# Optimization experiments

Measured on AMD Instinct MI355X. Metric: run time of the kernel, lower is better.

## Reference

```python
import jax, jax.numpy as jnp
import numpy as np

B, L, D_IN, D, P, NL = 8, 4096, 64, 512, 512, 3
EPS = 1e-5


def _ln(x, w, b):
    m = x.mean(-1, keepdims=True)
    v = ((x - m) ** 2).mean(-1, keepdims=True)
    return (x - m) * jax.lax.rsqrt(v + EPS) * w + b


def _gelu(x):
    return jax.nn.gelu(x, approximate=False)  # torch default = exact erf GELU


def _s5_scan(u, lam_re, lam_im, Bre, Bim, Cre, Cim, Dp, log_step):
    # u: (L, D). Diagonal complex SSM with ZOH discretization.
    lam = lam_re + 1j * lam_im                      # (P,)
    step = jnp.exp(log_step)                        # (P,)
    lam_bar = jnp.exp(lam * step)                   # (P,)
    Bt = Bre + 1j * Bim                             # (P, D)
    B_bar = ((lam_bar - 1.0) / lam)[:, None] * Bt   # (P, D)
    Bu = u.astype(jnp.complex64) @ B_bar.T          # (L, P)
    A = jnp.broadcast_to(lam_bar, Bu.shape)         # (L, P)

    def binop(a, b):
        A1, b1 = a
        A2, b2 = b
        return (A2 * A1, A2 * b1 + b2)

    _, xs = jax.lax.associative_scan(binop, (A, Bu))  # (L, P) states
    Ct = Cre + 1j * Cim                               # (D, P)
    return 2.0 * jnp.real(xs @ Ct.T) + Dp * u          # (L, D)


def setup_inputs() -> dict:
    key = jax.random.key(0)
    ks = iter(jax.random.split(key, 32))
    r = lambda s, sc=1.0: sc * jax.random.normal(next(ks), s, dtype=jnp.float32)
    inp = {}
    inp['x'] = r((B, L, D_IN))
    inp['lengths'] = jax.random.randint(next(ks), (B,), 1, L + 1, dtype=jnp.int32)
    inp['enc_w'] = r((D_IN, D), 0.05)
    inp['enc_b'] = jnp.zeros((D,), jnp.float32)
    # S5 SSM params per layer (stacked over NL)
    inp['lam_re'] = -jnp.exp(r((NL, P), 0.5))          # stable: Re(Lambda) < 0
    inp['lam_im'] = np.pi * r((NL, P))
    inp['Bre'] = r((NL, P, D), 1.0 / np.sqrt(D))
    inp['Bim'] = r((NL, P, D), 1.0 / np.sqrt(D))
    inp['Cre'] = r((NL, D, P), 1.0 / np.sqrt(P))
    inp['Cim'] = r((NL, D, P), 1.0 / np.sqrt(P))
    inp['Dp'] = r((NL, D))
    inp['log_step'] = jax.random.uniform(next(ks), (NL, P), jnp.float32, np.log(1e-3), np.log(1e-1))
    # S5Block norms and GEGLU FFN (ff_enc: D->2D no bias, ff_dec: D->D no bias)
    inp['an_w'] = jnp.ones((NL, D), jnp.float32)
    inp['an_b'] = jnp.zeros((NL, D), jnp.float32)
    inp['fn_w'] = jnp.ones((NL, D), jnp.float32)
    inp['fn_b'] = jnp.zeros((NL, D), jnp.float32)
    inp['ffe_w'] = r((NL, 2 * D, D), 1.0 / np.sqrt(D))
    inp['ffd_w'] = r((NL, D, D), 1.0 / np.sqrt(D))
    # outer prenorm LayerNorms
    inp['norm_w'] = jnp.ones((NL, D), jnp.float32)
    inp['norm_b'] = jnp.zeros((NL, D), jnp.float32)
    inp['head_w'] = r((1, D), 0.05)
    inp['head_b'] = jnp.zeros((1,), jnp.float32)
    return inp


def reference(x, lengths, enc_w, enc_b, lam_re, lam_im, Bre, Bim, Cre, Cim, Dp,
              log_step, an_w, an_b, fn_w, fn_b, ffe_w, ffd_w, norm_w, norm_b,
              head_w, head_b):
    h = x @ enc_w + enc_b  # (B, L, D)
    s5_b = jax.vmap(_s5_scan, in_axes=(0, None, None, None, None, None, None, None, None))
    for i in range(NL):
        z = _ln(h, norm_w[i], norm_b[i])  # prenorm (dropout = identity in eval)
        # --- S5Block ---
        fx = _ln(z, an_w[i], an_b[i])
        z = _gelu(s5_b(fx, lam_re[i], lam_im[i], Bre[i], Bim[i], Cre[i], Cim[i], Dp[i], log_step[i])) + fx
        fx = _ln(z, fn_w[i], fn_b[i])
        e = fx @ ffe_w[i].T                      # (B, L, 2D)
        a, g = jnp.split(e, 2, axis=-1)
        z = (a * _gelu(g)) @ ffd_w[i].T + fx      # GEGLU + residual
        h = h + z
    mask = (jnp.arange(L)[None, :] < lengths[:, None])[..., None]  # (B, L, 1)
    pooled = (h * mask).sum(axis=1) / jnp.maximum(lengths, 1)[:, None].astype(h.dtype)
    return (pooled @ head_w.T + head_b).squeeze(-1)  # (B,)
```

## Files before the change

kernel.cpp:

```cpp
#include <hip/hip_runtime.h>
#include <hip/hip_bf16.h>
#include <stdint.h>

#define BB 8
#define LL 4096
#define D_IN 64
#define DD 512
#define PP 512
#define NL 3
#define MTOK (BB * LL)
#define SCHUNK 128
#define NCHUNK (LL / SCHUNK)

typedef __bf16 bf16x8 __attribute__((ext_vector_type(8)));
typedef __bf16 bf16x4 __attribute__((ext_vector_type(4)));
typedef float f32x4 __attribute__((ext_vector_type(4)));

typedef const __attribute__((address_space(1))) void gvoid_t;
typedef __attribute__((address_space(3))) void svoid_t;

__device__ __forceinline__ void async16(const __bf16* g, __bf16* l) {
    __builtin_amdgcn_global_load_lds((gvoid_t*)g, (svoid_t*)l, 16, 0, 0);
}

__device__ __forceinline__ float gelu_f(float x) {
    return 0.5f * x * (1.0f + erff(x * 0.70710678118654752440f));
}
__device__ __forceinline__ float wred(float v) {
#pragma unroll
    for (int o = 32; o > 0; o >>= 1) v += __shfl_xor(v, o, 64);
    return v;
}
__device__ __forceinline__ float bflo(uint32_t u) { return __builtin_bit_cast(float, (uint32_t)(u << 16)); }
__device__ __forceinline__ float bfhi(uint32_t u) { return __builtin_bit_cast(float, (uint32_t)(u & 0xffff0000u)); }
__device__ __forceinline__ uint32_t packbf2(float a, float b) {
    unsigned short ha = __builtin_bit_cast(unsigned short, (__bf16)a);
    unsigned short hb = __builtin_bit_cast(unsigned short, (__bf16)b);
    return (uint32_t)ha | ((uint32_t)hb << 16);
}
__device__ __forceinline__ float ldf(const void* p, long i, int f) {
    return f ? ((const float*)p)[i] : (float)((const __bf16*)p)[i];
}
__device__ __forceinline__ void split1(float v, __bf16& h, __bf16& l) {
    h = (__bf16)v;
    l = (__bf16)(v - (float)h);
}

__global__ void detect(const uint32_t* __restrict__ an_w_raw, int* __restrict__ flag) {
    if (threadIdx.x == 0) *flag = (an_w_raw[0] == 0x3F800000u) ? 1 : 0;
}

template <bool AL, bool BL>
__device__ __forceinline__ void gemm_kloop(
    const __bf16* __restrict__ Ah, const __bf16* __restrict__ Al,
    const __bf16* __restrict__ Bh, const __bf16* __restrict__ Bl,
    long ga, long gb, int lda, int K,
    __bf16* dAh, __bf16* dAl, __bf16* dBh, __bf16* dBl,
    const __bf16* sAh, const __bf16* sAl, const __bf16* sBh, const __bf16* sBl,
    int wm, int wn, int fr, int co, f32x4 (&acc)[4][4])
{
    constexpr int HB = 16384;

    auto stage = [&](int boff, int k0) {
        async16(Ah + ga + k0, dAh + boff);
        async16(Ah + ga + k0 + 16 * (long)lda, dAh + boff + 512);
        if constexpr (AL) {
            async16(Al + ga + k0, dAl + boff);
            async16(Al + ga + k0 + 16 * (long)lda, dAl + boff + 512);
        }
        async16(Bh + gb + k0, dBh + boff);
        async16(Bh + gb + k0 + 16 * (long)K, dBh + boff + 512);
        if constexpr (BL) {
            async16(Bl + gb + k0, dBl + boff);
            async16(Bl + gb + k0 + 16 * (long)K, dBl + boff + 512);
        }
    };

    stage(0, 0);
    asm volatile("s_waitcnt vmcnt(0)" ::: "memory");
    __builtin_amdgcn_s_barrier();
    __builtin_amdgcn_sched_barrier(0);

    int roff = 0;
    for (int k0 = 0; k0 < K; k0 += 32) {
        if (k0 + 32 < K) stage(roff ^ HB, k0 + 32);

        bf16x8 afh[4], afl[4], bfh[4], bfl[4];
#pragma unroll
        for (int i = 0; i < 4; i++) {
            afh[i] = *(const bf16x8*)(sAh + roff + (wm * 64 + i * 16 + fr) * 32 + co);
            bfh[i] = *(const bf16x8*)(sBh + roff + (wn * 64 + i * 16 + fr) * 32 + co);
            if constexpr (AL) afl[i] = *(const bf16x8*)(sAl + roff + (wm * 64 + i * 16 + fr) * 32 + co);
            if constexpr (BL) bfl[i] = *(const bf16x8*)(sBl + roff + (wn * 64 + i * 16 + fr) * 32 + co);
        }
#pragma unroll
        for (int i = 0; i < 4; i++)
#pragma unroll
            for (int j = 0; j < 4; j++) {
                if constexpr (BL)
                    acc[i][j] = __builtin_amdgcn_mfma_f32_16x16x32_bf16(afh[i], bfl[j], acc[i][j], 0, 0, 0);
                if constexpr (AL)
                    acc[i][j] = __builtin_amdgcn_mfma_f32_16x16x32_bf16(afl[i], bfh[j], acc[i][j], 0, 0, 0);
                acc[i][j] = __builtin_amdgcn_mfma_f32_16x16x32_bf16(afh[i], bfh[j], acc[i][j], 0, 0, 0);
            }

        asm volatile("s_waitcnt vmcnt(0) lgkmcnt(0)" ::: "memory");
        __builtin_amdgcn_s_barrier();
        __builtin_amdgcn_sched_barrier(0);
        roff ^= HB;
    }
}

template <int MODE, bool ARAW, bool BRAW>
__global__ __launch_bounds__(256) void gemm_bt(
    const __bf16* __restrict__ Ah, const __bf16* __restrict__ Al, int lda,
    const __bf16* __restrict__ Bh, const __bf16* __restrict__ Bl,
    int M, int N, int K,
    __bf16* outh, __bf16* outl, float* h32,
    __bf16* fxh, __bf16* fxl, const float* __restrict__ vec,
    const int* __restrict__ lengths, float* __restrict__ partials, int b0,
    const int* __restrict__ flag)
{
    __shared__ __attribute__((aligned(16))) char smem[65536];
    __bf16* sAh = (__bf16*)smem;
    __bf16* sAl = (__bf16*)(smem + 8192);
    __bf16* sBh = (__bf16*)(smem + 16384);
    __bf16* sBl = (__bf16*)(smem + 24576);

    const int tid = threadIdx.x;
    const int lane = tid & 63;
    const int wave = tid >> 6;
    const int wm = wave & 1, wn = wave >> 1;
    const long m0 = (long)blockIdx.x * 128;
    const long n0 = (long)blockIdx.y * 128;

    f32x4 acc[4][4] = {};

    const int sr = lane >> 2;
    const int sc = ((lane & 3) ^ ((sr >> 1) & 3)) * 8;
    const long ga = (m0 + wave * 32 + sr) * (long)lda + sc;
    const long gb = (n0 + wave * 32 + sr) * (long)K + sc;
    __bf16* dAh = sAh + wave * 1024;
    __bf16* dAl = sAl + wave * 1024;
    __bf16* dBh = sBh + wave * 1024;
    __bf16* dBl = sBl + wave * 1024;

    const int fr = lane & 15;
    const int co = ((lane >> 4) ^ ((fr >> 1) & 3)) * 8;

    if constexpr (!ARAW && !BRAW) {
        gemm_kloop<true, true>(Ah, Al, Bh, Bl, ga, gb, lda, K, dAh, dAl, dBh, dBl,
                               sAh, sAl, sBh, sBl, wm, wn, fr, co, acc);
    } else {
        const int f32ds = *flag;
        if (f32ds) {
            gemm_kloop<true, true>(Ah, Al, Bh, Bl, ga, gb, lda, K, dAh, dAl, dBh, dBl,
                                   sAh, sAl, sBh, sBl, wm, wn, fr, co, acc);
        } else if constexpr (ARAW && BRAW) {
            gemm_kloop<false, false>(Ah, Al, Bh, Bl, ga, gb, lda, K, dAh, dAl, dBh, dBl,
                                     sAh, sAl, sBh, sBl, wm, wn, fr, co, acc);
        } else if constexpr (!ARAW && BRAW) {
            gemm_kloop<true, false>(Ah, Al, Bh, Bl, ga, gb, lda, K, dAh, dAl, dBh, dBl,
                                    sAh, sAl, sBh, sBl, wm, wn, fr, co, acc);
        } else {
            gemm_kloop<false, true>(Ah, Al, Bh, Bl, ga, gb, lda, K, dAh, dAl, dBh, dBl,
                                    sAh, sAl, sBh, sBl, wm, wn, fr, co, acc);
        }
    }

    float* scratch = (float*)smem + wave * 1088;
    const int er = (lane >> 4) * 4;
    const int ec = lane & 15;
    const int lr_rd = lane >> 3;
    const int lc_rd = (lane & 7) * 8;

    float pacc = 0.f;
    int lenb = 0;
    if (MODE == 5) lenb = lengths[b0 + (int)(blockIdx.x >> 5)];

#pragma unroll
    for (int i = 0; i < 4; i++) {
#pragma unroll
        for (int j = 0; j < 4; j++)
#pragma unroll
            for (int r = 0; r < 4; r++)
                scratch[(er + r) * 68 + j * 16 + ec] = acc[i][j][r];
#pragma unroll
        for (int s = 0; s < 2; s++) {
            const int lr = s * 8 + lr_rd;
            float v8[8];
            *(f32x4*)v8       = *(const f32x4*)&scratch[lr * 68 + lc_rd];
            *(f32x4*)(v8 + 4) = *(const f32x4*)&scratch[lr * 68 + lc_rd + 4];
            const long gm = m0 + wm * 64 + i * 16 + lr;
            const int gc = (int)n0 + wn * 64 + lc_rd;
            if (MODE == 0) {
                const long idx = gm * N + gc;
                bf16x8 h8, l8;
#pragma unroll
                for (int e = 0; e < 8; e++) { __bf16 h, l; split1(v8[e], h, l); h8[e] = h; l8[e] = l; }
                *(bf16x8*)(outh + idx) = h8;
                *(bf16x8*)(outl + idx) = l8;
            } else if (MODE == 1) {
                const long idx = gm * N + gc;
                f32x4 o0, o1;
#pragma unroll
                for (int e = 0; e < 4; e++) { o0[e] = v8[e] + vec[gc + e]; o1[e] = v8[4 + e] + vec[gc + 4 + e]; }
                *(f32x4*)(h32 + idx) = o0;
                *(f32x4*)(h32 + idx + 4) = o1;
            } else if (MODE == 2) {
                const long idx = gm * N + gc;
                const bf16x8 uh = *(const bf16x8*)(fxh + idx);
                const bf16x8 ul = *(const bf16x8*)(fxl + idx);
                bf16x8 h8, l8;
#pragma unroll
                for (int e = 0; e < 8; e++) {
                    const float u = (float)uh[e] + (float)ul[e];
                    const float z = gelu_f(v8[e] + vec[gc + e] * u) + u;
                    __bf16 h, l; split1(z, h, l); h8[e] = h; l8[e] = l;
                }
                *(bf16x8*)(fxh + idx) = h8;
                *(bf16x8*)(fxl + idx) = l8;
            } else if (MODE == 3 || MODE == 5) {
                const long idx = gm * N + gc;
                const bf16x8 uh = *(const bf16x8*)(fxh + idx);
                const bf16x8 ul = *(const bf16x8*)(fxl + idx);
                f32x4 o0 = *(const f32x4*)(h32 + idx);
                f32x4 o1 = *(const f32x4*)(h32 + idx + 4);
#pragma unroll
                for (int e = 0; e < 4; e++) {
                    o0[e] += v8[e] + (float)uh[e] + (float)ul[e];
                    o1[e] += v8[4 + e] + (float)uh[4 + e] + (float)ul[4 + e];
                }
                if (MODE == 3) {
                    *(f32x4*)(h32 + idx) = o0;
                    *(f32x4*)(h32 + idx + 4) = o1;
                } else {
                    if ((int)(gm & (LL - 1)) < lenb) {
#pragma unroll
                        for (int e = 0; e < 4; e++)
                            pacc += o0[e] * vec[gc + e] + o1[e] * vec[gc + 4 + e];
                    }
                }
            } else {
                const long tidx = gm * (N / 2) + (gc >> 1);
                bf16x4 h4, l4;
#pragma unroll
                for (int q = 0; q < 4; q++) {
                    const float t = v8[2 * q] * gelu_f(v8[2 * q + 1]);
                    __bf16 h, l; split1(t, h, l); h4[q] = h; l4[q] = l;
                }
                *(bf16x4*)(outh + tidx) = h4;
                *(bf16x4*)(outl + tidx) = l4;
            }
        }
    }

    if (MODE == 5) {
        pacc = wred(pacc);
        float* red = (float*)(smem + 17408);
        if (lane == 0) red[wave] = pacc;
        __syncthreads();
        if (tid == 0)
            partials[(long)(b0 + (int)(blockIdx.x >> 5)) * 128 +
                     (int)(blockIdx.x & 31) * 4 + (int)blockIdx.y] =
                red[0] + red[1] + red[2] + red[3];
    }
}

template <bool DBL, bool F32IN>
__global__ __launch_bounds__(256) void ln_kernel(
    const float* __restrict__ xf, const __bf16* xh, const __bf16* xl,
    __bf16* oh, __bf16* ol,
    const float* __restrict__ w1, const float* __restrict__ b1,
    const float* __restrict__ w2, const float* __restrict__ b2)
{
    const int lane = threadIdx.x & 63;
    const int wave = threadIdx.x >> 6;
    const long row = (long)blockIdx.x * 4 + wave;
    const int c0 = lane * 8;

    float v[8];
    if (F32IN) {
        const float* xp = xf + row * DD + c0;
        const float4 a = *(const float4*)xp;
        const float4 b = *(const float4*)(xp + 4);
        v[0] = a.x; v[1] = a.y; v[2] = a.z; v[3] = a.w;
        v[4] = b.x; v[5] = b.y; v[6] = b.z; v[7] = b.w;
    } else {
        const bf16x8 a = *(const bf16x8*)(xh + row * DD + c0);
        const bf16x8 b = *(const bf16x8*)(xl + row * DD + c0);
#pragma unroll
        for (int j = 0; j < 8; j++) v[j] = (float)a[j] + (float)b[j];
    }

    float s = 0.f;
#pragma unroll
    for (int j = 0; j < 8; j++) s += v[j];
    s = wred(s);
    float m = s * (1.0f / DD);
    float q = 0.f;
#pragma unroll
    for (int j = 0; j < 8; j++) { const float d = v[j] - m; q += d * d; }
    q = wred(q);
    float rstd = rsqrtf(q * (1.0f / DD) + 1e-5f);
    float y[8];
#pragma unroll
    for (int j = 0; j < 8; j++)
        y[j] = (v[j] - m) * rstd * w1[c0 + j] + b1[c0 + j];

    if (DBL) {
        s = 0.f;
#pragma unroll
        for (int j = 0; j < 8; j++) s += y[j];
        s = wred(s);
        m = s * (1.0f / DD);
        q = 0.f;
#pragma unroll
        for (int j = 0; j < 8; j++) { const float d = y[j] - m; q += d * d; }
        q = wred(q);
        rstd = rsqrtf(q * (1.0f / DD) + 1e-5f);
#pragma unroll
        for (int j = 0; j < 8; j++)
            y[j] = (y[j] - m) * rstd * w2[c0 + j] + b2[c0 + j];
    }

    bf16x8 oh8, ol8;
#pragma unroll
    for (int j = 0; j < 8; j++) { __bf16 h, l; split1(y[j], h, l); oh8[j] = h; ol8[j] = l; }
    *(bf16x8*)(oh + row * DD + c0) = oh8;
    *(bf16x8*)(ol + row * DD + c0) = ol8;
}

__global__ void prep_small(const void* enc_w, __bf16* __restrict__ eh, __bf16* __restrict__ el,
                           const void* lam_re, const void* lam_im, const void* logst,
                           float2* __restrict__ lamb, float2* __restrict__ abars,
                           float2* __restrict__ coef,
                           const void* nw, const void* nb, const void* aw, const void* ab,
                           const void* fw, const void* fb, const void* dp,
                           const void* eb, const void* hw, const void* hb,
                           float* __restrict__ cv, const int* __restrict__ flag)
{
    const int idx = blockIdx.x * 256 + threadIdx.x;
    const int f = *flag;
    {
        const int n = idx >> 6, k = idx & 63;
        __bf16 h, l;
        split1(ldf(enc_w, (long)k * DD + n, f), h, l);
        eh[idx] = h; el[idx] = l;
    }
    if (idx < NL * PP) {
        const float lre = ldf(lam_re, idx, f), lim = ldf(lam_im, idx, f);
        const float st = expf(ldf(logst, idx, f));
        const float ea = expf(lre * st);
        const float ang = lim * st;
        const float br = ea * cosf(ang), bi = ea * sinf(ang);
        lamb[idx] = make_float2(br, bi);
        float ar = br, ai = bi;
#pragma unroll
        for (int q = 0; q < 7; q++) { const float t = ar * ar - ai * ai; ai = 2.f * ar * ai; ar = t; }
        abars[idx] = make_float2(ar, ai);
        const float nr = br - 1.f, ni = bi;
        const float den = lre * lre + lim * lim;
        coef[idx] = make_float2((nr * lre + ni * lim) / den, (ni * lre - nr * lim) / den);
    }
    const int NV = NL * DD;
    if (idx < 7 * NV + 1025) {
        if (idx < NV) cv[idx] = ldf(nw, idx, f);
        else if (idx < 2 * NV) cv[idx] = ldf(nb, idx - NV, f);
        else if (idx < 3 * NV) cv[idx] = ldf(aw, idx - 2 * NV, f);
        else if (idx < 4 * NV) cv[idx] = ldf(ab, idx - 3 * NV, f);
        else if (idx < 5 * NV) cv[idx] = ldf(fw, idx - 4 * NV, f);
        else if (idx < 6 * NV) cv[idx] = ldf(fb, idx - 5 * NV, f);
        else if (idx < 7 * NV) cv[idx] = ldf(dp, idx - 6 * NV, f);
        else if (idx < 7 * NV + 512) cv[idx] = ldf(eb, idx - 7 * NV, f);
        else if (idx < 7 * NV + 1024) cv[idx] = ldf(hw, idx - 7 * NV - 512, f);
        else cv[idx] = ldf(hb, idx - 7 * NV - 1024, f);
    }
}

__global__ void prep_w12(const void* Bre, const void* Bim, const float2* __restrict__ coef,
                         __bf16* __restrict__ W1th, __bf16* __restrict__ W1tl,
                         const void* Cre, const void* Cim,
                         __bf16* __restrict__ W2th, __bf16* __restrict__ W2tl,
                         const int* __restrict__ flag)
{
    const long idx = (long)blockIdx.x * 256 + threadIdx.x;
    const int f = *flag;
    const long li = idx >> 18;
    const int pd = (int)(idx & ((1 << 18) - 1));
    {
        const int p = pd >> 9, d = pd & 511;
        const float2 c = coef[li * PP + p];
        const float br = ldf(Bre, idx, f), bi = ldf(Bim, idx, f);
        const float re = c.x * br - c.y * bi;
        const float im = c.x * bi + c.y * br;
        const long base = li * (2 * PP) * DD;
        __bf16 h, l;
        split1(re, h, l); W1th[base + (long)(2 * p) * DD + d] = h; W1tl[base + (long)(2 * p) * DD + d] = l;
        split1(im, h, l); W1th[base + (long)(2 * p + 1) * DD + d] = h; W1tl[base + (long)(2 * p + 1) * DD + d] = l;
    }
    {
        const int d = pd >> 9, p = pd & 511;
        const long base = li * DD * (2 * PP);
        __bf16 h, l;
        split1(2.f * ldf(Cre, idx, f), h, l);
        W2th[base + (long)d * (2 * PP) + 2 * p] = h; W2tl[base + (long)d * (2 * PP) + 2 * p] = l;
        split1(-2.f * ldf(Cim, idx, f), h, l);
        W2th[base + (long)d * (2 * PP) + 2 * p + 1] = h; W2tl[base + (long)d * (2 * PP) + 2 * p + 1] = l;
    }
}

__global__ void prep_ff(const void* ffe, __bf16* __restrict__ feh, __bf16* __restrict__ fel,
                        const void* ffd, __bf16* __restrict__ fdh, __bf16* __restrict__ fdl,
                        const int* __restrict__ flag)
{
    const long idx = (long)blockIdx.x * 256 + threadIdx.x;
    const int f = *flag;
    {
        const long li = idx >> 19;
        const int rc = (int)(idx & ((1 << 19) - 1));
        const int r = rc >> 9, c = rc & 511;
        const int nr = (r < 512) ? (2 * r) : (2 * (r - 512) + 1);
        __bf16 h, l;
        split1(ldf(ffe, idx, f), h, l);
        const long dst = li * (1 << 19) + (long)nr * 512 + c;
        feh[dst] = h; fel[dst] = l;
    }
    if (idx < (long)NL * DD * DD) {
        __bf16 h, l;
        split1(ldf(ffd, idx, f), h, l);
        fdh[idx] = h; fdl[idx] = l;
    }
}

__global__ void split_arr(const void* src, __bf16* __restrict__ dh, __bf16* __restrict__ dl,
                          long n, const int* __restrict__ flag)
{
    const long idx = (long)blockIdx.x * 256 + threadIdx.x;
    if (idx >= n) return;
    __bf16 h, l;
    split1(ldf(src, idx, *flag), h, l);
    dh[idx] = h; dl[idx] = l;
}

__global__ __launch_bounds__(256) void scan_ends(const uint32_t* __restrict__ wh32,
                                                 const uint32_t* __restrict__ wl32,
                                                 const float2* __restrict__ lamb,
                                                 float2* __restrict__ ends)
{
    const int idx = blockIdx.x * 256 + threadIdx.x;
    const int p = idx & 511;
    const int c = (idx >> 9) & (NCHUNK - 1);
    const int b = idx >> 14;
    const float2 lb = lamb[p];
    const long base = ((long)(b * LL + c * SCHUNK)) * 512 + p;
    float sr = 0.f, si = 0.f;
    for (int j = 0; j < SCHUNK; j++) {
        const uint32_t uh = wh32[base + (long)j * 512];
        const uint32_t ul = wl32[base + (long)j * 512];
        const float br = bflo(uh) + bflo(ul);
        const float bi = bfhi(uh) + bfhi(ul);
        const float ns = fmaf(lb.x, sr, fmaf(-lb.y, si, br));
        si = fmaf(lb.x, si, fmaf(lb.y, sr, bi));
        sr = ns;
    }
    ends[((long)(b * PP + p)) * NCHUNK + c] = make_float2(sr, si);
}

__global__ __launch_bounds__(256) void scan_carry(const float2* __restrict__ abars,
                                                  float2* __restrict__ ends)
{
    const int idx = blockIdx.x * 256 + threadIdx.x;
    const int p = idx & 511;
    const float2 As = abars[p];
    float2* eb = ends + (long)idx * NCHUNK;
    float cr = 0.f, ci = 0.f;
    for (int c = 0; c < NCHUNK; c++) {
        const float2 e = eb[c];
        eb[c] = make_float2(cr, ci);
        const float nr = As.x * cr - As.y * ci + e.x;
        ci = As.x * ci + As.y * cr + e.y;
        cr = nr;
    }
}

__global__ __launch_bounds__(256) void scan_fix(uint32_t* wh32, uint32_t* wl32,
                                                const float2* __restrict__ lamb,
                                                const float2* __restrict__ ends)
{
    const int idx = blockIdx.x * 256 + threadIdx.x;
    const int p = idx & 511;
    const int c = (idx >> 9) & (NCHUNK - 1);
    const int b = idx >> 14;
    const float2 lb = lamb[p];
    const float2 carry = ends[((long)(b * PP + p)) * NCHUNK + c];
    const long base = ((long)(b * LL + c * SCHUNK)) * 512 + p;
    float sr = carry.x, si = carry.y;
    for (int j = 0; j < SCHUNK; j++) {
        const uint32_t uh = wh32[base + (long)j * 512];
        const uint32_t ul = wl32[base + (long)j * 512];
        const float br = bflo(uh) + bflo(ul);
        const float bi = bfhi(uh) + bfhi(ul);
        const float ns = fmaf(lb.x, sr, fmaf(-lb.y, si, br));
        si = fmaf(lb.x, si, fmaf(lb.y, sr, bi));
        sr = ns;
        const float hr = (float)(__bf16)sr, hi_ = (float)(__bf16)si;
        wh32[base + (long)j * 512] = packbf2(sr, si);
        wl32[base + (long)j * 512] = packbf2(sr - hr, si - hi_);
    }
}

__global__ void pool2(const float* __restrict__ partials, const int* __restrict__ lengths,
                      const float* __restrict__ hb_, void* out, const int* __restrict__ flag)
{
    const int b = threadIdx.x;
    if (b >= BB) return;
    float s = 0.f;
    for (int c = 0; c < 128; c++) s += partials[b * 128 + c];
    const int len = lengths[b] < 1 ? 1 : lengths[b];
    const float val = s / (float)len + hb_[0];
    if (*flag) ((float*)out)[b] = val;
    else ((__bf16*)out)[b] = (__bf16)val;
}

extern "C" void kernel_launch(void* const* d_in, const int* in_sizes, int n_in,
                              void* d_out, int out_size, void* d_ws, size_t ws_size,
                              hipStream_t stream)
{
    const void* x      = d_in[0];
    const int* lengths = (const int*)d_in[1];
    const void* enc_w  = d_in[2];
    const void* enc_b  = d_in[3];
    const void* lam_re = d_in[4];
    const void* lam_im = d_in[5];
    const void* Bre    = d_in[6];
    const void* Bim    = d_in[7];
    const void* Cre    = d_in[8];
    const void* Cim    = d_in[9];
    const void* Dp     = d_in[10];
    const void* logst  = d_in[11];
    const void* an_w   = d_in[12];
    const void* an_b   = d_in[13];
    const void* fn_w   = d_in[14];
    const void* fn_b   = d_in[15];
    const void* ffe    = d_in[16];
    const void* ffd    = d_in[17];
    const void* norm_w = d_in[18];
    const void* norm_b = d_in[19];
    const void* head_w = d_in[20];
    const void* head_b = d_in[21];

    char* w = (char*)d_ws;
    auto alloc = [&](size_t bytes) -> char* {
        char* r = w;
        w += (bytes + 255) & ~(size_t)255;
        return r;
    };
    int* dflag    = (int*)alloc(256);
    __bf16* W1th  = (__bf16*)alloc((size_t)NL * 2 * PP * DD * 2);
    __bf16* W1tl  = (__bf16*)alloc((size_t)NL * 2 * PP * DD * 2);
    __bf16* W2th  = (__bf16*)alloc((size_t)NL * DD * 2 * PP * 2);
    __bf16* W2tl  = (__bf16*)alloc((size_t)NL * DD * 2 * PP * 2);
    __bf16* ffeh  = (__bf16*)alloc((size_t)NL * 2 * DD * DD * 2);
    __bf16* ffel  = (__bf16*)alloc((size_t)NL * 2 * DD * DD * 2);
    __bf16* ffdh  = (__bf16*)alloc((size_t)NL * DD * DD * 2);
    __bf16* ffdl  = (__bf16*)alloc((size_t)NL * DD * DD * 2);
    __bf16* ench  = (__bf16*)alloc((size_t)DD * D_IN * 2);
    __bf16* encl  = (__bf16*)alloc((size_t)DD * D_IN * 2);
    __bf16* xh    = (__bf16*)alloc((size_t)MTOK * D_IN * 2);
    __bf16* xl    = (__bf16*)alloc((size_t)MTOK * D_IN * 2);
    float2* lamb  = (float2*)alloc((size_t)NL * PP * 8);
    float2* abars = (float2*)alloc((size_t)NL * PP * 8);
    float2* coef  = (float2*)alloc((size_t)NL * PP * 8);
    float*  cv    = (float*)alloc((size_t)(7 * NL * DD + 1025) * 4);
    float2* ends  = (float2*)alloc((size_t)BB * PP * NCHUNK * 8);
    float* partials = (float*)alloc((size_t)BB * 128 * 4);
    const size_t fixed = (size_t)(w - (char*)d_ws);

    int NB = BB;
    const size_t per_b = (size_t)LL * DD * 16;
    while (NB > 1 && fixed + (size_t)NB * per_b > ws_size) NB >>= 1;
    float* h32  = (float*)alloc((size_t)NB * LL * DD * 4);
    __bf16* fxh = (__bf16*)alloc((size_t)NB * LL * DD * 2);
    __bf16* fxl = (__bf16*)alloc((size_t)NB * LL * DD * 2);
    __bf16* wh  = (__bf16*)alloc((size_t)NB * LL * 2 * PP * 2);
    __bf16* wl  = (__bf16*)alloc((size_t)NB * LL * 2 * PP * 2);

    const float* cv_nw = cv;
    const float* cv_nb = cv + 1536;
    const float* cv_aw = cv + 3072;
    const float* cv_ab = cv + 4608;
    const float* cv_fw = cv + 6144;
    const float* cv_fb = cv + 7680;
    const float* cv_dp = cv + 9216;
    const float* cv_eb = cv + 10752;
    const float* cv_hw = cv + 11264;
    const float* cv_hb = cv + 11776;

    detect<<<1, 64, 0, stream>>>((const uint32_t*)an_w, dflag);
    prep_small<<<128, 256, 0, stream>>>(enc_w, ench, encl, lam_re, lam_im, logst,
                                        lamb, abars, coef,
                                        norm_w, norm_b, an_w, an_b, fn_w, fn_b, Dp,
                                        enc_b, head_w, head_b, cv, dflag);
    prep_w12<<<(NL * PP * DD) / 256, 256, 0, stream>>>(
        Bre, Bim, coef, W1th, W1tl, Cre, Cim, W2th, W2tl, dflag);
    prep_ff<<<((size_t)NL * 2 * DD * DD) / 256, 256, 0, stream>>>(
        ffe, ffeh, ffel, ffd, ffdh, ffdl, dflag);
    split_arr<<<((size_t)MTOK * D_IN + 255) / 256, 256, 0, stream>>>(
        x, xh, xl, (long)MTOK * D_IN, dflag);

    for (int b0 = 0; b0 < BB; b0 += NB) {
        const int M = NB * LL;
        gemm_bt<1, true, true><<<dim3(M / 128, DD / 128), 256, 0, stream>>>(
            xh + (long)b0 * LL * D_IN, xl + (long)b0 * LL * D_IN, D_IN,
            ench, encl, M, DD, D_IN, nullptr, nullptr, h32, nullptr, nullptr, cv_eb,
            nullptr, nullptr, 0, dflag);

        for (int li = 0; li < NL; li++) {
            ln_kernel<true, true><<<M / 4, 256, 0, stream>>>(
                h32, nullptr, nullptr, fxh, fxl,
                cv_nw + li * DD, cv_nb + li * DD, cv_aw + li * DD, cv_ab + li * DD);
            gemm_bt<0, false, false><<<dim3(M / 128, (2 * PP) / 128), 256, 0, stream>>>(
                fxh, fxl, DD, W1th + (long)li * 2 * PP * DD, W1tl + (long)li * 2 * PP * DD,
                M, 2 * PP, DD, wh, wl, nullptr, nullptr, nullptr, nullptr,
                nullptr, nullptr, 0, dflag);
            scan_ends<<<(NB * NCHUNK * PP) / 256, 256, 0, stream>>>(
                (const uint32_t*)wh, (const uint32_t*)wl, lamb + li * PP, ends);
            scan_carry<<<(NB * PP) / 256, 256, 0, stream>>>(abars + li * PP, ends);
            scan_fix<<<(NB * NCHUNK * PP) / 256, 256, 0, stream>>>(
                (uint32_t*)wh, (uint32_t*)wl, lamb + li * PP, ends);
            gemm_bt<2, false, true><<<dim3(M / 128, DD / 128), 256, 0, stream>>>(
                wh, wl, 2 * PP, W2th + (long)li * DD * 2 * PP, W2tl + (long)li * DD * 2 * PP,
                M, DD, 2 * PP, nullptr, nullptr, nullptr, fxh, fxl, cv_dp + li * DD,
                nullptr, nullptr, 0, dflag);
            ln_kernel<false, false><<<M / 4, 256, 0, stream>>>(
                nullptr, fxh, fxl, fxh, fxl,
                cv_fw + li * DD, cv_fb + li * DD, nullptr, nullptr);
            gemm_bt<4, false, true><<<dim3(M / 128, (2 * DD) / 128), 256, 0, stream>>>(
                fxh, fxl, DD, ffeh + (long)li * 2 * DD * DD, ffel + (long)li * 2 * DD * DD,
                M, 2 * DD, DD, wh, wl, nullptr, nullptr, nullptr, nullptr,
                nullptr, nullptr, 0, dflag);
            if (li < NL - 1) {
                gemm_bt<3, false, true><<<dim3(M / 128, DD / 128), 256, 0, stream>>>(
                    wh, wl, DD, ffdh + (long)li * DD * DD, ffdl + (long)li * DD * DD,
                    M, DD, DD, nullptr, nullptr, h32, fxh, fxl, nullptr,
                    nullptr, nullptr, 0, dflag);
            } else {
                gemm_bt<5, false, true><<<dim3(M / 128, DD / 128), 256, 0, stream>>>(
                    wh, wl, DD, ffdh + (long)li * DD * DD, ffdl + (long)li * DD * DD,
                    M, DD, DD, nullptr, nullptr, h32, fxh, fxl, cv_hw,
                    lengths, partials, b0, dflag);
            }
        }
    }
    pool2<<<1, 64, 0, stream>>>(partials, lengths, cv_hb, d_out, dflag);
}
```

Before: 1.950 ms.

## Fold scan carry pass into scan_fix and halve scan chunk length

Removes the separate scan_carry kernel. Each scan_fix thread now recomputes its incoming carry by serially combining the preceding chunk-end states, read from an ends buffer relaid out as (b, chunk, p) so those reads coalesce. The chunk length drops from 128 to 64, so there are twice as many chunks and the serial inner loops are shorter, which exposes more parallelism. In exchange, carry work is redundant (up to 63 extra complex FMAs per thread) and one kernel launch plus a serial low-parallelism pass is eliminated.

```diff
diff --git a/kernel.cpp b/kernel.cpp
--- a/kernel.cpp
+++ b/kernel.cpp
@@ -9,8 +9,10 @@
 #define PP 512
 #define NL 3
 #define MTOK (BB * LL)
-#define SCHUNK 128
+#define SCHUNK 64
+#define SCHUNK_LOG 6
 #define NCHUNK (LL / SCHUNK)
+#define NCHUNK_LOG 6
 
 typedef __bf16 bf16x8 __attribute__((ext_vector_type(8)));
 typedef __bf16 bf16x4 __attribute__((ext_vector_type(4)));
@@ -357,7 +359,7 @@
         lamb[idx] = make_float2(br, bi);
         float ar = br, ai = bi;
 #pragma unroll
-        for (int q = 0; q < 7; q++) { const float t = ar * ar - ai * ai; ai = 2.f * ar * ai; ar = t; }
+        for (int q = 0; q < SCHUNK_LOG; q++) { const float t = ar * ar - ai * ai; ai = 2.f * ar * ai; ar = t; }
         abars[idx] = make_float2(ar, ai);
         const float nr = br - 1.f, ni = bi;
         const float den = lre * lre + lim * lim;
@@ -451,7 +453,7 @@
     const int idx = blockIdx.x * 256 + threadIdx.x;
     const int p = idx & 511;
     const int c = (idx >> 9) & (NCHUNK - 1);
-    const int b = idx >> 14;
+    const int b = idx >> (9 + NCHUNK_LOG);
     const float2 lb = lamb[p];
     const long base = ((long)(b * LL + c * SCHUNK)) * 512 + p;
     float sr = 0.f, si = 0.f;
@@ -464,38 +466,32 @@
         si = fmaf(lb.x, si, fmaf(lb.y, sr, bi));
         sr = ns;
     }
-    ends[((long)(b * PP + p)) * NCHUNK + c] = make_float2(sr, si);
-}
-
-__global__ __launch_bounds__(256) void scan_carry(const float2* __restrict__ abars,
-                                                  float2* __restrict__ ends)
-{
-    const int idx = blockIdx.x * 256 + threadIdx.x;
-    const int p = idx & 511;
-    const float2 As = abars[p];
-    float2* eb = ends + (long)idx * NCHUNK;
-    float cr = 0.f, ci = 0.f;
-    for (int c = 0; c < NCHUNK; c++) {
-        const float2 e = eb[c];
-        eb[c] = make_float2(cr, ci);
-        const float nr = As.x * cr - As.y * ci + e.x;
-        ci = As.x * ci + As.y * cr + e.y;
-        cr = nr;
-    }
+    ends[((long)b * NCHUNK + c) * PP + p] = make_float2(sr, si);
 }
 
 __global__ __launch_bounds__(256) void scan_fix(uint32_t* wh32, uint32_t* wl32,
                                                 const float2* __restrict__ lamb,
+                                                const float2* __restrict__ abars,
                                                 const float2* __restrict__ ends)
 {
     const int idx = blockIdx.x * 256 + threadIdx.x;
     const int p = idx & 511;
     const int c = (idx >> 9) & (NCHUNK - 1);
-    const int b = idx >> 14;
+    const int b = idx >> (9 + NCHUNK_LOG);
     const float2 lb = lamb[p];
-    const float2 carry = ends[((long)(b * PP + p)) * NCHUNK + c];
+
+    const float2 As = abars[p];
+    const float2* eb = ends + (long)b * NCHUNK * PP + p;
+    float cr = 0.f, ci = 0.f;
+    for (int cc = 0; cc < c; cc++) {
+        const float2 e = eb[(long)cc * PP];
+        const float nr = fmaf(As.x, cr, fmaf(-As.y, ci, e.x));
+        ci = fmaf(As.x, ci, fmaf(As.y, cr, e.y));
+        cr = nr;
+    }
+
     const long base = ((long)(b * LL + c * SCHUNK)) * 512 + p;
-    float sr = carry.x, si = carry.y;
+    float sr = cr, si = ci;
     for (int j = 0; j < SCHUNK; j++) {
         const uint32_t uh = wh32[base + (long)j * 512];
         const uint32_t ul = wl32[base + (long)j * 512];
@@ -626,9 +622,8 @@
                 nullptr, nullptr, 0, dflag);
             scan_ends<<<(NB * NCHUNK * PP) / 256, 256, 0, stream>>>(
                 (const uint32_t*)wh, (const uint32_t*)wl, lamb + li * PP, ends);
-            scan_carry<<<(NB * PP) / 256, 256, 0, stream>>>(abars + li * PP, ends);
             scan_fix<<<(NB * NCHUNK * PP) / 256, 256, 0, stream>>>(
-                (uint32_t*)wh, (uint32_t*)wl, lamb + li * PP, ends);
+                (uint32_t*)wh, (uint32_t*)wl, lamb + li * PP, abars + li * PP, ends);
             gemm_bt<2, false, true><<<dim3(M / 128, DD / 128), 256, 0, stream>>>(
                 wh, wl, 2 * PP, W2th + (long)li * DD * 2 * PP, W2tl + (long)li * DD * 2 * PP,
                 M, DD, 2 * PP, nullptr, nullptr, nullptr, fxh, fxl, cv_dp + li * DD,
```

New measurement: 1.846 ms. 5.4% less time.
